# Performance work log

Measured on AMD Instinct MI355X. Metric: run time of the kernel, lower is better.

## Reference

```python
import jax, jax.numpy as jnp
import numpy as np

C, N, G = 10, 500000, 8


def setup_inputs() -> dict:
    key = jax.random.key(0)
    k1, k2 = jax.random.split(key)
    group_act = jax.random.uniform(k1, (C, N, G), dtype=jnp.float32)
    target_labels = jax.random.randint(k2, (N,), 0, 11, dtype=jnp.int64 if jax.config.jax_enable_x64 else jnp.int32)
    return {"group_act": group_act, "target_labels": target_labels}


def reference(group_act, target_labels):
    # group_act: [C, N, G] (stacked list_group_activation), target_labels: [N] in 0..C (0 => ignored)
    labels = target_labels.reshape(-1) - 1                      # [N], -1 => skip
    c, n, g = group_act.shape
    masks = (labels[None, :] == jnp.arange(c)[:, None]).astype(group_act.dtype)  # [C, N]
    counts = masks.sum(axis=1)                                  # [C]
    valid = counts >= 2                                         # classes actually contributing

    Am = group_act * masks[:, :, None]                          # [C, N, G] masked activations
    col_sum = Am.sum(axis=1)                                    # [C, G]
    p = Am / col_sum[:, None, :]                                # normalized per column (zero on unmasked rows)
    # log only over masked rows (original indexes rows by cls_mask before log)
    m3 = masks[:, :, None] > 0
    logp = jnp.where(m3, jnp.log(jnp.where(m3, p, 1.0)), 0.0)   # [C, N, G]

    # M[c, i, j] = sum_n p[c,n,i] * log p[c,n,j]; loss_ij = -M[c,i,j] for i != j
    M = jnp.einsum('cni,cnj->cij', p, logp)                     # [C, G, G]
    offdiag = M * (1.0 - jnp.eye(g, dtype=M.dtype))
    per_class = offdiag.sum(axis=(1, 2))                        # [C]

    num = jnp.sum(jnp.where(valid, per_class, 0.0))
    denom = jnp.sum(valid.astype(M.dtype)) * (g * (g - 1))
    # original: tot = mean(-M_ij); return -tot == mean(M_ij)
    return num / denom
```

## Files before the change

### kernel.cpp

```cpp
#include <hip/hip_runtime.h>

#define C_CLS 10
#define G_DIM 8


__global__ void k_init(float* cs, int* counts, float* total) {
    int t = threadIdx.x;
    if (t < C_CLS * G_DIM) cs[t] = 0.0f;
    if (t < C_CLS) counts[t] = 0;
    if (t == 0) *total = 0.0f;
}

__global__ void k_colsum(const float* __restrict__ ga, const int* __restrict__ lbl,
                         float* __restrict__ g_cs, int* __restrict__ g_counts, int N) {
    __shared__ float s_cs[C_CLS * G_DIM];
    __shared__ int s_cnt[C_CLS];
    int t = threadIdx.x;
    if (t < C_CLS * G_DIM) s_cs[t] = 0.0f;
    if (t < C_CLS) s_cnt[t] = 0;
    __syncthreads();

    int stride = gridDim.x * blockDim.x;
    for (int n = blockIdx.x * blockDim.x + t; n < N; n += stride) {
        int l = lbl[n];
        if (l > 0) {
            int c = l - 1;
            const float4* row = (const float4*)(ga + ((size_t)c * N + n) * G_DIM);
            float4 v0 = row[0];
            float4 v1 = row[1];
            atomicAdd(&s_cnt[c], 1);
            float* b = &s_cs[c * G_DIM];
            atomicAdd(&b[0], v0.x);
            atomicAdd(&b[1], v0.y);
            atomicAdd(&b[2], v0.z);
            atomicAdd(&b[3], v0.w);
            atomicAdd(&b[4], v1.x);
            atomicAdd(&b[5], v1.y);
            atomicAdd(&b[6], v1.z);
            atomicAdd(&b[7], v1.w);
        }
    }
    __syncthreads();
    if (t < C_CLS * G_DIM) atomicAdd(&g_cs[t], s_cs[t]);
    if (t < C_CLS) atomicAdd(&g_counts[t], s_cnt[t]);
}

__global__ void k_loss(const float* __restrict__ ga, const int* __restrict__ lbl,
                       const float* __restrict__ g_cs, const int* __restrict__ g_counts,
                       float* __restrict__ g_total, int N) {
    __shared__ float s_inv[C_CLS * G_DIM];
    __shared__ float s_lcs[C_CLS * G_DIM];
    __shared__ float s_val[C_CLS];
    int t = threadIdx.x;
    if (t < C_CLS * G_DIM) {
        float cs = g_cs[t];
        s_inv[t] = 1.0f / cs;
        s_lcs[t] = __logf(cs);
    }
    if (t < C_CLS) s_val[t] = (g_counts[t] >= 2) ? 1.0f : 0.0f;
    __syncthreads();

    float acc = 0.0f;
    int stride = gridDim.x * blockDim.x;
    for (int n = blockIdx.x * blockDim.x + t; n < N; n += stride) {
        int l = lbl[n];
        if (l > 0) {
            int c = l - 1;
            const float4* row = (const float4*)(ga + ((size_t)c * N + n) * G_DIM);
            float4 v0 = row[0];
            float4 v1 = row[1];
            float a[G_DIM] = {v0.x, v0.y, v0.z, v0.w, v1.x, v1.y, v1.z, v1.w};
            const float* inv = &s_inv[c * G_DIM];
            const float* lcs = &s_lcs[c * G_DIM];
            float S = 0.0f, L = 0.0f, D = 0.0f;
#pragma unroll
            for (int g = 0; g < G_DIM; ++g) {
                float s = a[g] * inv[g];
                float lg = __logf(a[g]) - lcs[g];
                S += s;
                L += lg;
                D += s * lg;
            }
            acc += s_val[c] * (S * L - D);
        }
    }

#pragma unroll
    for (int off = 32; off > 0; off >>= 1) acc += __shfl_down(acc, off, 64);
    __shared__ float s_red[4];
    int wid = t >> 6, lid = t & 63;
    if (lid == 0) s_red[wid] = acc;
    __syncthreads();
    if (t == 0) {
        atomicAdd(g_total, s_red[0] + s_red[1] + s_red[2] + s_red[3]);
    }
}

__global__ void k_fin(const int* __restrict__ counts, const float* __restrict__ total,
                      float* __restrict__ out) {
    if (threadIdx.x == 0) {
        int nv = 0;
        for (int c = 0; c < C_CLS; ++c) nv += (counts[c] >= 2) ? 1 : 0;
        out[0] = total[0] / ((float)nv * (float)(G_DIM * (G_DIM - 1)));
    }
}

extern "C" void kernel_launch(void* const* d_in, const int* in_sizes, int n_in,
                              void* d_out, int out_size, void* d_ws, size_t ws_size,
                              hipStream_t stream) {
    const float* ga = (const float*)d_in[0];
    const int* lbl = (const int*)d_in[1];
    float* out = (float*)d_out;
    int N = in_sizes[1];

    char* ws = (char*)d_ws;
    float* cs = (float*)ws;
    int* counts = (int*)(ws + 320);
    float* total = (float*)(ws + 360);

    k_init<<<1, 128, 0, stream>>>(cs, counts, total);
    k_colsum<<<1024, 256, 0, stream>>>(ga, lbl, cs, counts, N);
    k_loss<<<1024, 256, 0, stream>>>(ga, lbl, cs, counts, total, N);
    k_fin<<<1, 64, 0, stream>>>(counts, total, out);
}
```

Before: 244.2 us.

## Fuse colsum and loss into one dense per-class pass via algebraic decomposition

Rewrites the loss so each class needs only per-column sums of a, a*sum(log a) and a*log a, plus a count. The log column sums are then applied once in the final kernel. This lets a single kernel stream each class plane densely, with a (chunk, class) grid, register accumulators and wave reductions. It replaces two gather passes that did heavy shared-memory atomics. The price is reading all ten planes, about ten times the data, instead of only each row's labelled class, and possible fp32 cancellation from subtracting large accumulated sums.

```diff
diff --git a/kernel.cpp b/kernel.cpp
--- a/kernel.cpp
+++ b/kernel.cpp
@@ -2,106 +2,104 @@
 
 #define C_CLS 10
 #define G_DIM 8
+#define CHUNKS 128
+#define ACC_W 26
 
-
-__global__ void k_init(float* cs, int* counts, float* total) {
+__global__ void k_init(float* acc) {
     int t = threadIdx.x;
-    if (t < C_CLS * G_DIM) cs[t] = 0.0f;
-    if (t < C_CLS) counts[t] = 0;
-    if (t == 0) *total = 0.0f;
+    if (t < C_CLS * ACC_W) acc[t] = 0.0f;
 }
 
-__global__ void k_colsum(const float* __restrict__ ga, const int* __restrict__ lbl,
-                         float* __restrict__ g_cs, int* __restrict__ g_counts, int N) {
-    __shared__ float s_cs[C_CLS * G_DIM];
-    __shared__ int s_cnt[C_CLS];
-    int t = threadIdx.x;
-    if (t < C_CLS * G_DIM) s_cs[t] = 0.0f;
-    if (t < C_CLS) s_cnt[t] = 0;
-    __syncthreads();
-
-    int stride = gridDim.x * blockDim.x;
-    for (int n = blockIdx.x * blockDim.x + t; n < N; n += stride) {
-        int l = lbl[n];
-        if (l > 0) {
-            int c = l - 1;
-            const float4* row = (const float4*)(ga + ((size_t)c * N + n) * G_DIM);
-            float4 v0 = row[0];
-            float4 v1 = row[1];
-            atomicAdd(&s_cnt[c], 1);
-            float* b = &s_cs[c * G_DIM];
-            atomicAdd(&b[0], v0.x);
-            atomicAdd(&b[1], v0.y);
-            atomicAdd(&b[2], v0.z);
-            atomicAdd(&b[3], v0.w);
-            atomicAdd(&b[4], v1.x);
-            atomicAdd(&b[5], v1.y);
-            atomicAdd(&b[6], v1.z);
-            atomicAdd(&b[7], v1.w);
-        }
-    }
-    __syncthreads();
-    if (t < C_CLS * G_DIM) atomicAdd(&g_cs[t], s_cs[t]);
-    if (t < C_CLS) atomicAdd(&g_counts[t], s_cnt[t]);
+__device__ inline float wave_red(float v) {
+#pragma unroll
+    for (int off = 32; off > 0; off >>= 1) v += __shfl_down(v, off, 64);
+    return v;
 }
 
-__global__ void k_loss(const float* __restrict__ ga, const int* __restrict__ lbl,
-                       const float* __restrict__ g_cs, const int* __restrict__ g_counts,
-                       float* __restrict__ g_total, int N) {
-    __shared__ float s_inv[C_CLS * G_DIM];
-    __shared__ float s_lcs[C_CLS * G_DIM];
-    __shared__ float s_val[C_CLS];
-    int t = threadIdx.x;
-    if (t < C_CLS * G_DIM) {
-        float cs = g_cs[t];
-        s_inv[t] = 1.0f / cs;
-        s_lcs[t] = __logf(cs);
-    }
-    if (t < C_CLS) s_val[t] = (g_counts[t] >= 2) ? 1.0f : 0.0f;
-    __syncthreads();
+__global__ void __launch_bounds__(256) k_main(const float* __restrict__ ga,
+                                              const int* __restrict__ lbl,
+                                              float* __restrict__ g_acc, int N) {
+    const int c = blockIdx.y;
+    const int chunk_len = (N + CHUNKS - 1) / CHUNKS;
+    const int base = blockIdx.x * chunk_len;
+    const int end = min(base + chunk_len, N);
 
-    float acc = 0.0f;
-    int stride = gridDim.x * blockDim.x;
-    for (int n = blockIdx.x * blockDim.x + t; n < N; n += stride) {
+    float cs_a[G_DIM], R_a[G_DIM], D_a[G_DIM];
+#pragma unroll
+    for (int g = 0; g < G_DIM; ++g) { cs_a[g] = 0.0f; R_a[g] = 0.0f; D_a[g] = 0.0f; }
+    float cnt = 0.0f;
+
+    const float* plane = ga + (size_t)c * N * G_DIM;
+    for (int n = base + (int)threadIdx.x; n < end; n += blockDim.x) {
+        const float4* row = (const float4*)(plane + (size_t)n * G_DIM);
+        float4 v0 = row[0];
+        float4 v1 = row[1];
         int l = lbl[n];
-        if (l > 0) {
-            int c = l - 1;
-            const float4* row = (const float4*)(ga + ((size_t)c * N + n) * G_DIM);
-            float4 v0 = row[0];
-            float4 v1 = row[1];
-            float a[G_DIM] = {v0.x, v0.y, v0.z, v0.w, v1.x, v1.y, v1.z, v1.w};
-            const float* inv = &s_inv[c * G_DIM];
-            const float* lcs = &s_lcs[c * G_DIM];
-            float S = 0.0f, L = 0.0f, D = 0.0f;
+        float m = (l == c + 1) ? 1.0f : 0.0f;
+        float a[G_DIM] = {v0.x, v0.y, v0.z, v0.w, v1.x, v1.y, v1.z, v1.w};
+        float la[G_DIM];
+        float L = 0.0f;
 #pragma unroll
-            for (int g = 0; g < G_DIM; ++g) {
-                float s = a[g] * inv[g];
-                float lg = __logf(a[g]) - lcs[g];
-                S += s;
-                L += lg;
-                D += s * lg;
-            }
-            acc += s_val[c] * (S * L - D);
+        for (int g = 0; g < G_DIM; ++g) {
+            la[g] = __logf(fmaxf(a[g], 1e-30f));
+            L += la[g];
+        }
+        cnt += m;
+#pragma unroll
+        for (int g = 0; g < G_DIM; ++g) {
+            float am = a[g] * m;
+            cs_a[g] += am;
+            R_a[g] = fmaf(am, L, R_a[g]);
+            D_a[g] = fmaf(am, la[g], D_a[g]);
         }
     }
 
 #pragma unroll
-    for (int off = 32; off > 0; off >>= 1) acc += __shfl_down(acc, off, 64);
-    __shared__ float s_red[4];
-    int wid = t >> 6, lid = t & 63;
-    if (lid == 0) s_red[wid] = acc;
+    for (int g = 0; g < G_DIM; ++g) {
+        cs_a[g] = wave_red(cs_a[g]);
+        R_a[g] = wave_red(R_a[g]);
+        D_a[g] = wave_red(D_a[g]);
+    }
+    cnt = wave_red(cnt);
+
+    __shared__ float s_part[4][ACC_W];
+    int wid = threadIdx.x >> 6, lid = threadIdx.x & 63;
+    if (lid == 0) {
+#pragma unroll
+        for (int g = 0; g < G_DIM; ++g) {
+            s_part[wid][g] = cs_a[g];
+            s_part[wid][8 + g] = R_a[g];
+            s_part[wid][16 + g] = D_a[g];
+        }
+        s_part[wid][24] = cnt;
+    }
     __syncthreads();
-    if (t == 0) {
-        atomicAdd(g_total, s_red[0] + s_red[1] + s_red[2] + s_red[3]);
+    int t = threadIdx.x;
+    if (t < ACC_W - 1) {
+        float v = s_part[0][t] + s_part[1][t] + s_part[2][t] + s_part[3][t];
+        atomicAdd(&g_acc[c * ACC_W + t], v);
     }
 }
 
-__global__ void k_fin(const int* __restrict__ counts, const float* __restrict__ total,
-                      float* __restrict__ out) {
+__global__ void k_fin(const float* __restrict__ acc, float* __restrict__ out) {
     if (threadIdx.x == 0) {
+        float tot = 0.0f;
         int nv = 0;
-        for (int c = 0; c < C_CLS; ++c) nv += (counts[c] >= 2) ? 1 : 0;
-        out[0] = total[0] / ((float)nv * (float)(G_DIM * (G_DIM - 1)));
+        for (int c = 0; c < C_CLS; ++c) {
+            const float* a = acc + c * ACC_W;
+            float cnt = a[24];
+            if (cnt >= 2.0f) {
+                nv++;
+                float Lc = 0.0f, s = 0.0f;
+                for (int i = 0; i < G_DIM; ++i) {
+                    float cs = a[i];
+                    Lc += __logf(cs);
+                    s += (a[8 + i] - a[16 + i]) / cs;
+                }
+                tot += s - (float)(G_DIM - 1) * Lc;
+            }
+        }
+        out[0] = tot / ((float)nv * (float)(G_DIM * (G_DIM - 1)));
     }
 }
 
@@ -113,13 +111,10 @@
     float* out = (float*)d_out;
     int N = in_sizes[1];
 
-    char* ws = (char*)d_ws;
-    float* cs = (float*)ws;
-    int* counts = (int*)(ws + 320);
-    float* total = (float*)(ws + 360);
+    float* acc = (float*)d_ws;
 
-    k_init<<<1, 128, 0, stream>>>(cs, counts, total);
-    k_colsum<<<1024, 256, 0, stream>>>(ga, lbl, cs, counts, N);
-    k_loss<<<1024, 256, 0, stream>>>(ga, lbl, cs, counts, total, N);
-    k_fin<<<1, 64, 0, stream>>>(counts, total, out);
+    k_init<<<1, 512, 0, stream>>>(acc);
+    dim3 grid(CHUNKS, C_CLS);
+    k_main<<<grid, 256, 0, stream>>>(ga, lbl, acc, N);
+    k_fin<<<1, 64, 0, stream>>>(acc, out);
 }
```

Measured after the change: 241.7 us. About the same (-1.0%).
